# Performance work log

Hardware: AMD Instinct MI355X
Metric: run time of the kernel (lower is better)

## Reference

```python
import jax, jax.numpy as jnp
import numpy as np

B, S, NX, H = 8, 1024, 1024, 16
HD = NX // H  # head dim = 64
MASKED_BIAS = -10000.0


def setup_inputs() -> dict:
    key = jax.random.key(0)
    ks = jax.random.split(key, 6)
    return {
        "x": jax.random.normal(ks[0], (B, S, NX), dtype=jnp.float32),
        "query": jax.random.normal(ks[1], (B, S, NX), dtype=jnp.float32),
        "c_attn_w": jax.random.normal(ks[2], (NX, 3 * NX), dtype=jnp.float32) * 0.02,
        "c_attn_b": jnp.zeros((3 * NX,), dtype=jnp.float32),
        "c_proj_w": jax.random.normal(ks[3], (NX, NX), dtype=jnp.float32) * 0.02,
        "c_proj_b": jnp.zeros((NX,), dtype=jnp.float32),
    }


def _split_heads(t):
    # [B, S, NX] -> [B, H, S, HD]
    b, s, _ = t.shape
    return t.reshape(b, s, H, HD).transpose(0, 2, 1, 3)


def reference(x, query, c_attn_w, c_attn_b, c_proj_w, c_proj_b):
    # Conv1D: y = x @ W + b
    kv = x @ c_attn_w + c_attn_b          # [B,S,3NX]; use key/value slices
    qy = query @ c_attn_w + c_attn_b      # [B,S,3NX]; use query slice
    q = _split_heads(qy[..., :NX])                     # [B,H,S,HD]
    k = _split_heads(kv[..., NX:2 * NX])               # [B,H,S,HD]
    v = _split_heads(kv[..., 2 * NX:])                 # [B,H,S,HD]

    w = jnp.einsum("bhqd,bhkd->bhqk", q, k) / jnp.sqrt(jnp.float32(HD))
    causal = jnp.tril(jnp.ones((S, S), dtype=bool))[None, None]
    w = jnp.where(causal, w, jnp.float32(MASKED_BIAS))
    w = jax.nn.softmax(w, axis=-1)
    a = jnp.einsum("bhqk,bhkd->bhqd", w, v)            # [B,H,S,HD]
    a = a.transpose(0, 2, 1, 3).reshape(B, S, NX)      # merge heads
    return a @ c_proj_w + c_proj_b
```

## Files before the change

kernel.cpp:

```cpp
#include <hip/hip_runtime.h>
#include <cstdint>
#include <cstddef>

#define Bb   8
#define Ss   1024
#define NXx  1024
#define Hh   16
#define HDd  64
#define Mm   (Bb*Ss)

typedef __bf16 bf16x8 __attribute__((ext_vector_type(8)));
typedef float  f32x4  __attribute__((ext_vector_type(4)));

__device__ __forceinline__ unsigned short f2bf(float f) {
    union { float f; unsigned int u; } v; v.f = f;
    return (unsigned short)((v.u + 0x8000u) >> 16);
}
__device__ __forceinline__ unsigned int f2bf_hi(float f) {
    union { float f; unsigned int u; } v; v.f = f;
    return (v.u + 0x8000u) & 0xffff0000u;
}

__device__ __forceinline__ void load_lds16(const unsigned short* g, unsigned short* lds_base) {
    __builtin_amdgcn_global_load_lds(
        (const __attribute__((address_space(1))) void*)g,
        (__attribute__((address_space(3))) void*)lds_base, 16, 0, 0);
}

__global__ __launch_bounds__(256) void prep(
    const float* __restrict__ x, const float* __restrict__ query,
    const float* __restrict__ caw, const float* __restrict__ cpw,
    unsigned short* __restrict__ xb, unsigned short* __restrict__ qb,
    unsigned short* __restrict__ Wt, unsigned short* __restrict__ Pt)
{
    __shared__ float tile[32][33];
    const int bid = blockIdx.x;
    const int tid = threadIdx.x;

    if (bid < 16384) {
        const float* in = (bid < 8192) ? x : query;
        unsigned short* out = (bid < 8192) ? xb : qb;
        const int i = ((bid & 8191) * 256 + tid) * 4;
        const float4 v = *(const float4*)(in + i);
        unsigned long long p = (unsigned long long)f2bf(v.x)
            | ((unsigned long long)f2bf(v.y) << 16)
            | ((unsigned long long)f2bf(v.z) << 32)
            | ((unsigned long long)f2bf(v.w) << 48);
        *(unsigned long long*)(out + i) = p;
        return;
    }

    const float* in;
    unsigned short* out;
    int C, t;
    if (bid < 16384 + 3072) { in = caw; out = Wt; C = 3072; t = bid - 16384; }
    else                    { in = cpw; out = Pt; C = 1024; t = bid - 19456; }
    const int ntx = C >> 5;
    const int c0 = (t % ntx) * 32, r0 = (t / ntx) * 32;
    const int tx = tid & 31, ty = tid >> 5;
    for (int i = ty; i < 32; i += 8)
        tile[i][tx] = in[(size_t)(r0 + i) * C + c0 + tx];
    __syncthreads();
    for (int i = ty; i < 32; i += 8)
        out[(size_t)(c0 + i) * 1024 + r0 + tx] = f2bf(tile[tx][i]);
}

__global__ __launch_bounds__(256) void gemm128(
    const unsigned short* __restrict__ Ax,
    const unsigned short* __restrict__ Aq,
    const unsigned short* __restrict__ Bt,
    const float* __restrict__ bias,
    int K, int mode,
    unsigned short* __restrict__ out_q,
    unsigned short* __restrict__ out_k,
    unsigned short* __restrict__ out_v,
    float* __restrict__ out_f)
{
    __shared__ unsigned short smem[16384];
    unsigned short (*As)[64] = (unsigned short (*)[64])(smem);
    unsigned short (*Bs)[64] = (unsigned short (*)[64])(smem + 8192);

    const int tid  = threadIdx.x;
    const int w    = tid >> 6;
    const int lane = tid & 63;

    const int nx   = (mode == 0) ? 24 : 8;
    const int nxh  = nx >> 1;
    const int n    = blockIdx.x;
    const int xcd  = n & 7;
    const int sgrp = n >> 3;
    const int m0   = ((xcd >> 1) * 16 + sgrp / nxh) * 128;
    const int n0   = ((xcd & 1) * nxh + sgrp % nxh) * 128;
    const int region = n0 >> 10;
    const unsigned short* A = (mode == 0 && region == 0) ? Aq : Ax;

    const int wm   = (w >> 1) * 64;
    const int wn   = (w & 1) * 64;
    const int lrow = lane & 15;
    const int quad = lane >> 4;

    f32x4 acc[4][4] = {};

    const int rr   = lane >> 3;
    const int scol = (((lane & 7) ^ (lane >> 3)) << 3);
    const unsigned short* Ag = A  + (size_t)(m0 + w * 32 + rr) * K + scol;
    const unsigned short* Bg = Bt + (size_t)(n0 + w * 32 + rr) * K + scol;
    unsigned short* ldsA = smem + (w * 32) * 64;
    unsigned short* ldsB = smem + 8192 + (w * 32) * 64;

    const int swz = lrow & 7;

    for (int k0 = 0; k0 < K; k0 += 64) {
        __syncthreads();
#pragma unroll
        for (int c = 0; c < 4; ++c) {
            load_lds16(Ag + (size_t)(c * 8) * K + k0, ldsA + c * 512);
            load_lds16(Bg + (size_t)(c * 8) * K + k0, ldsB + c * 512);
        }
        __syncthreads();
#pragma unroll
        for (int kk = 0; kk < 2; ++kk) {
            bf16x8 af[4], bfr[4];
            const int pc = (((kk * 4 + quad) ^ swz) << 3);
#pragma unroll
            for (int i = 0; i < 4; ++i) {
                af[i]  = *(const bf16x8*)&As[wm + i * 16 + lrow][pc];
                bfr[i] = *(const bf16x8*)&Bs[wn + i * 16 + lrow][pc];
            }
#pragma unroll
            for (int i = 0; i < 4; ++i)
#pragma unroll
                for (int j = 0; j < 4; ++j)
                    acc[i][j] = __builtin_amdgcn_mfma_f32_16x16x32_bf16(af[i], bfr[j], acc[i][j], 0, 0, 0);
        }
    }

    __syncthreads();

    if (mode == 1) {
#pragma unroll
        for (int i = 0; i < 4; ++i)
#pragma unroll
            for (int j = 0; j < 4; ++j) {
                const int ncol = n0 + wn + j * 16 + lrow;
                const float bv = bias[ncol];
#pragma unroll
                for (int r = 0; r < 4; ++r) {
                    const int mrow = m0 + wm + i * 16 + quad * 4 + r;
                    out_f[(size_t)mrow * NXx + ncol] = acc[i][j][r] + bv;
                }
            }
        return;
    }

    unsigned short* ep = smem + w * 2048;

    if (region != 2) {
        unsigned short* outp = (region == 0) ? out_q : out_k;
#pragma unroll
        for (int j = 0; j < 4; ++j) {
            const float bv = bias[n0 + wn + j * 16 + lrow];
#pragma unroll
            for (int i = 0; i < 4; ++i)
#pragma unroll
                for (int r = 0; r < 4; ++r)
                    ep[(i * 16 + quad * 4 + r) * 24 + lrow] = f2bf(acc[i][j][r] + bv);
#pragma unroll
            for (int t = 0; t < 2; ++t) {
                const int c    = t * 64 + lane;
                const int row  = c >> 1, ch = (c & 1) * 8;
                const int mrow = m0 + wm + row;
                const int cc   = (n0 + wn + j * 16 + ch) & (NXx - 1);
                const int hh   = cc >> 6, dd = cc & 63;
                const int bh   = (mrow >> 10) * Hh + hh;
                const int ss   = mrow & (Ss - 1);
                *(uint4*)&outp[((size_t)bh * Ss + ss) * HDd + dd] =
                    *(const uint4*)&ep[row * 24 + ch];
            }
        }
    } else {
#pragma unroll
        for (int j = 0; j < 4; ++j) {
            const float bv = bias[n0 + wn + j * 16 + lrow];
#pragma unroll
            for (int i = 0; i < 4; ++i)
#pragma unroll
                for (int r = 0; r < 4; ++r)
                    ep[lrow * 72 + i * 16 + quad * 4 + r] = f2bf(acc[i][j][r] + bv);
#pragma unroll
            for (int t = 0; t < 2; ++t) {
                const int c    = t * 64 + lane;
                const int col  = c >> 3, rc = (c & 7) * 8;
                const int cc   = (n0 + wn + j * 16 + col) & (NXx - 1);
                const int hh   = cc >> 6, dd = cc & 63;
                const int mrow = m0 + wm + rc;
                const int bh   = (mrow >> 10) * Hh + hh;
                const int ss   = mrow & (Ss - 1);
                *(uint4*)&out_v[((size_t)bh * HDd + dd) * Ss + ss] =
                    *(const uint4*)&ep[col * 72 + rc];
            }
        }
    }
}

__global__ __launch_bounds__(512, 2) void gemm256(
    const unsigned short* __restrict__ Ax,
    const unsigned short* __restrict__ Aq,
    const unsigned short* __restrict__ Bt,
    const float* __restrict__ bias,
    unsigned short* __restrict__ out_q,
    unsigned short* __restrict__ out_k,
    unsigned short* __restrict__ out_v)
{
    __shared__ unsigned short lds[49152];

    const int tid  = threadIdx.x;
    const int w    = tid >> 6;
    const int lane = tid & 63;
    const int wm   = (w >> 2) * 128;
    const int wn   = (w & 3) * 32;
    const int lrow = lane & 15;
    const int quad = lane >> 4;
    const int swz  = lrow & 7;
    const int ca   = (quad ^ swz) << 3;
    const int cb   = ((4 + quad) ^ swz) << 3;

    const int n    = blockIdx.x;
    const int xcd  = n & 7;
    const int sg   = n >> 3;
    const int mi   = (xcd >> 1) * 8 + (sg & 7);
    const int ni   = (xcd & 1) * 12 + (sg >> 3);
    const int m0   = mi << 8;
    const int n0   = ni << 7;
    const int region = n0 >> 10;
    const unsigned short* A = (region == 0) ? Aq : Ax;

    const int srow = lane >> 3;
    const int chnk = (((lane & 7) ^ srow) << 3);
    const unsigned short* pA0 = A  + (size_t)(m0 +       w * 8 + srow) * 1024 + chnk;
    const unsigned short* pA1 = A  + (size_t)(m0 +  64 + w * 8 + srow) * 1024 + chnk;
    const unsigned short* pA2 = A  + (size_t)(m0 + 128 + w * 8 + srow) * 1024 + chnk;
    const unsigned short* pA3 = A  + (size_t)(m0 + 192 + w * 8 + srow) * 1024 + chnk;
    const unsigned short* pB0 = Bt + (size_t)(n0 +       w * 8 + srow) * 1024 + chnk;
    const unsigned short* pB1 = Bt + (size_t)(n0 +  64 + w * 8 + srow) * 1024 + chnk;
    const int wl = w * 512;

    f32x4 acc[8][2] = {};

    load_lds16(pA0, lds + 0 * 4096 + wl);
    load_lds16(pA2, lds + 2 * 4096 + wl);
    load_lds16(pB0, lds + 32768 + 0 * 4096 + wl);
    load_lds16(pB1, lds + 32768 + 1 * 4096 + wl);
    load_lds16(pA1, lds + 1 * 4096 + wl);
    load_lds16(pA3, lds + 3 * 4096 + wl);
    pA0 += 64; pA1 += 64; pA2 += 64; pA3 += 64;
    pB0 += 64; pB1 += 64;

    asm volatile("s_waitcnt vmcnt(2)" ::: "memory");
    __builtin_amdgcn_s_barrier();
    asm volatile("" ::: "memory");

#pragma unroll 1
    for (int t = 0; t < 16; ++t) {
        const int ab = (t & 1) * 16384;
        const int bb = 32768 + (t & 1) * 8192;
        const int ua = ((t & 1) ^ 1) * 16384;
        const int ub = 32768 + ((t & 1) ^ 1) * 8192;
        const bool st = (t < 15);
        const int rbA = ab + (wm + lrow) * 64;
        const int rbB = bb + (wn + lrow) * 64;

        bf16x8 a0f[4], a1f[4], b0q[2], b1q[2];

#pragma unroll
        for (int i = 0; i < 4; ++i) {
            a0f[i] = *(const bf16x8*)&lds[rbA + i * 1024 + ca];
            a1f[i] = *(const bf16x8*)&lds[rbA + i * 1024 + cb];
        }
#pragma unroll
        for (int j = 0; j < 2; ++j) {
            b0q[j] = *(const bf16x8*)&lds[rbB + j * 1024 + ca];
            b1q[j] = *(const bf16x8*)&lds[rbB + j * 1024 + cb];
        }
        if (st) {
            load_lds16(pA0, lds + ua + 0 * 4096 + wl);
            load_lds16(pA2, lds + ua + 2 * 4096 + wl);
            load_lds16(pB0, lds + ub + 0 * 4096 + wl);
            load_lds16(pB1, lds + ub + 1 * 4096 + wl);
        }
        __builtin_amdgcn_s_barrier();
        asm volatile("s_waitcnt lgkmcnt(0)" ::: "memory");
        __builtin_amdgcn_s_setprio(1);
#pragma unroll
        for (int i = 0; i < 4; ++i)
#pragma unroll
            for (int j = 0; j < 2; ++j)
                acc[i][j] = __builtin_amdgcn_mfma_f32_16x16x32_bf16(a0f[i], b0q[j], acc[i][j], 0, 0, 0);
#pragma unroll
        for (int i = 0; i < 4; ++i)
#pragma unroll
            for (int j = 0; j < 2; ++j)
                acc[i][j] = __builtin_amdgcn_mfma_f32_16x16x32_bf16(a1f[i], b1q[j], acc[i][j], 0, 0, 0);
        __builtin_amdgcn_s_setprio(0);
        if (st) asm volatile("s_waitcnt vmcnt(4)" ::: "memory");
        else    asm volatile("s_waitcnt vmcnt(0)" ::: "memory");
        asm volatile("" ::: "memory");
        __builtin_amdgcn_s_barrier();
        asm volatile("" ::: "memory");

#pragma unroll
        for (int i = 0; i < 4; ++i) {
            a0f[i] = *(const bf16x8*)&lds[rbA + 4096 + i * 1024 + ca];
            a1f[i] = *(const bf16x8*)&lds[rbA + 4096 + i * 1024 + cb];
        }
        if (st) {
            load_lds16(pA1, lds + ua + 1 * 4096 + wl);
            load_lds16(pA3, lds + ua + 3 * 4096 + wl);
            pA0 += 64; pA1 += 64; pA2 += 64; pA3 += 64;
            pB0 += 64; pB1 += 64;
        }
        __builtin_amdgcn_s_barrier();
        asm volatile("s_waitcnt lgkmcnt(0)" ::: "memory");
        __builtin_amdgcn_s_setprio(1);
#pragma unroll
        for (int i = 0; i < 4; ++i)
#pragma unroll
            for (int j = 0; j < 2; ++j)
                acc[4 + i][j] = __builtin_amdgcn_mfma_f32_16x16x32_bf16(a0f[i], b0q[j], acc[4 + i][j], 0, 0, 0);
#pragma unroll
        for (int i = 0; i < 4; ++i)
#pragma unroll
            for (int j = 0; j < 2; ++j)
                acc[4 + i][j] = __builtin_amdgcn_mfma_f32_16x16x32_bf16(a1f[i], b1q[j], acc[4 + i][j], 0, 0, 0);
        __builtin_amdgcn_s_setprio(0);
        if (st) asm volatile("s_waitcnt vmcnt(2)" ::: "memory");
        asm volatile("" ::: "memory");
        __builtin_amdgcn_s_barrier();
        asm volatile("" ::: "memory");
    }

    __syncthreads();

    unsigned short* ep = lds + w * 6144;

    if (region != 2) {
        unsigned short* outp = (region == 0) ? out_q : out_k;
#pragma unroll
        for (int j = 0; j < 2; ++j) {
            const float bv = bias[n0 + wn + j * 16 + lrow];
#pragma unroll
            for (int i = 0; i < 8; ++i)
#pragma unroll
                for (int r = 0; r < 4; ++r)
                    ep[(i * 16 + quad * 4 + r) * 24 + lrow] = f2bf(acc[i][j][r] + bv);
#pragma unroll
            for (int tt = 0; tt < 4; ++tt) {
                const int c    = tt * 64 + lane;
                const int row  = c >> 1, ch = (c & 1) * 8;
                const int mrow = m0 + wm + row;
                const int cc   = (n0 + wn + j * 16 + ch) & (NXx - 1);
                const int hh   = cc >> 6, dd = cc & 63;
                const int bh   = (mrow >> 10) * Hh + hh;
                const int ss   = mrow & (Ss - 1);
                *(uint4*)&outp[((size_t)bh * Ss + ss) * HDd + dd] =
                    *(const uint4*)&ep[row * 24 + ch];
            }
        }
    } else {
#pragma unroll
        for (int j = 0; j < 2; ++j) {
            const float bv = bias[n0 + wn + j * 16 + lrow];
#pragma unroll
            for (int i = 0; i < 8; ++i)
#pragma unroll
                for (int r = 0; r < 4; ++r)
                    ep[lrow * 136 + i * 16 + quad * 4 + r] = f2bf(acc[i][j][r] + bv);
#pragma unroll
            for (int tt = 0; tt < 4; ++tt) {
                const int c    = tt * 64 + lane;
                const int col  = c >> 4, rc = (c & 15) * 8;
                const int cc   = (n0 + wn + j * 16 + col) & (NXx - 1);
                const int hh   = cc >> 6, dd = cc & 63;
                const int mrow = m0 + wm + rc;
                const int bh   = (mrow >> 10) * Hh + hh;
                const int ss   = mrow & (Ss - 1);
                *(uint4*)&out_v[((size_t)bh * HDd + dd) * Ss + ss] =
                    *(const uint4*)&ep[col * 136 + rc];
            }
        }
    }
}

__global__ __launch_bounds__(256) void flash_attn(
    const unsigned short* __restrict__ Qh,
    const unsigned short* __restrict__ Kh,
    const unsigned short* __restrict__ Vt,
    unsigned short* __restrict__ about)
{
    __shared__ unsigned short Ks[64][64];
    __shared__ unsigned short Vs[64][64];
    __shared__ unsigned short Pl[4][32][72];

    const int tid  = threadIdx.x;
    const int w    = tid >> 6;
    const int lane = tid & 63;
    const int bh   = blockIdx.x & 127;
    const int pr   = blockIdx.x >> 7;
    const int b    = bh >> 4, h = bh & 15;
    const int lrow = lane & 15;
    const int quad = lane >> 4;

    const unsigned short* Qb = Qh + (size_t)bh * Ss * HDd;
    const unsigned short* Kb = Kh + (size_t)bh * Ss * HDd;
    const unsigned short* Vb = Vt + (size_t)bh * HDd * Ss;

    const int sr = lane >> 3;
    const int lc = (((lane & 7) ^ (lane >> 3)) << 3);
    unsigned short* ldsK0 = &Ks[w * 16][0];
    unsigned short* ldsK1 = &Ks[w * 16 + 8][0];
    unsigned short* ldsV0 = &Vs[w * 16][0];
    unsigned short* ldsV1 = &Vs[w * 16 + 8][0];

    const int swz = lrow & 7;
    const int ca = ((quad ^ swz) << 3);
    const int cb = (((4 + quad) ^ swz) << 3);

    for (int half = 0; half < 2; ++half) {
        const int qt = half ? (7 - pr) : pr;
        const int qw = qt * 128 + w * 32;

        bf16x8 aq[2][2];
#pragma unroll
        for (int g = 0; g < 2; ++g)
#pragma unroll
            for (int c = 0; c < 2; ++c)
                aq[g][c] = *(const bf16x8*)(Qb + (size_t)(qw + g * 16 + lrow) * HDd + c * 32 + quad * 8);

        f32x4 O[2][4] = {};
        float lsum[2] = { 0.f, 0.f };

        const int nkt = 2 * qt + 2;
        for (int kt = 0; kt < nkt; ++kt) {
            const int k0 = kt * 64;

            __syncthreads();
            load_lds16(Kb + (size_t)(k0 + w * 16 + sr) * HDd + lc,     ldsK0);
            load_lds16(Kb + (size_t)(k0 + w * 16 + sr + 8) * HDd + lc, ldsK1);
            load_lds16(Vb + (size_t)(w * 16 + sr) * Ss + k0 + lc,      ldsV0);
            load_lds16(Vb + (size_t)(w * 16 + sr + 8) * Ss + k0 + lc,  ldsV1);
            __syncthreads();

            if (k0 > qw + 31) continue;

            f32x4 st[2][4] = {};
#pragma unroll
            for (int j = 0; j < 4; ++j) {
                const bf16x8 kf0 = *(const bf16x8*)&Ks[j * 16 + lrow][ca];
                const bf16x8 kf1 = *(const bf16x8*)&Ks[j * 16 + lrow][cb];
                st[0][j] = __builtin_amdgcn_mfma_f32_16x16x32_bf16(kf0, aq[0][0], st[0][j], 0, 0, 0);
                st[0][j] = __builtin_amdgcn_mfma_f32_16x16x32_bf16(kf1, aq[0][1], st[0][j], 0, 0, 0);
                st[1][j] = __builtin_amdgcn_mfma_f32_16x16x32_bf16(kf0, aq[1][0], st[1][j], 0, 0, 0);
                st[1][j] = __builtin_amdgcn_mfma_f32_16x16x32_bf16(kf1, aq[1][1], st[1][j], 0, 0, 0);
            }

            const bool needMask = (k0 + 63 > qw);
#pragma unroll
            for (int g = 0; g < 2; ++g) {
                const int qg = qw + g * 16 + lrow;
#pragma unroll
                for (int j = 0; j < 4; ++j) {
                    const int kbase = k0 + j * 16 + quad * 4;
                    float e0 = __expf(st[g][j][0] * 0.125f);
                    float e1 = __expf(st[g][j][1] * 0.125f);
                    float e2 = __expf(st[g][j][2] * 0.125f);
                    float e3 = __expf(st[g][j][3] * 0.125f);
                    if (needMask) {
                        if (kbase     > qg) e0 = 0.f;
                        if (kbase + 1 > qg) e1 = 0.f;
                        if (kbase + 2 > qg) e2 = 0.f;
                        if (kbase + 3 > qg) e3 = 0.f;
                    }
                    lsum[g] += (e0 + e1) + (e2 + e3);
                    uint2 pk;
                    pk.x = (unsigned)f2bf(e0) | f2bf_hi(e1);
                    pk.y = (unsigned)f2bf(e2) | f2bf_hi(e3);
                    *(uint2*)&Pl[w][g * 16 + lrow][j * 16 + quad * 4] = pk;
                }
            }

            bf16x8 ap[2][2];
#pragma unroll
            for (int g = 0; g < 2; ++g)
#pragma unroll
                for (int c = 0; c < 2; ++c)
                    ap[g][c] = *(const bf16x8*)&Pl[w][g * 16 + lrow][c * 32 + quad * 8];
#pragma unroll
            for (int f = 0; f < 4; ++f) {
                const bf16x8 vf0 = *(const bf16x8*)&Vs[f * 16 + lrow][ca];
                const bf16x8 vf1 = *(const bf16x8*)&Vs[f * 16 + lrow][cb];
                O[0][f] = __builtin_amdgcn_mfma_f32_16x16x32_bf16(ap[0][0], vf0, O[0][f], 0, 0, 0);
                O[0][f] = __builtin_amdgcn_mfma_f32_16x16x32_bf16(ap[0][1], vf1, O[0][f], 0, 0, 0);
                O[1][f] = __builtin_amdgcn_mfma_f32_16x16x32_bf16(ap[1][0], vf0, O[1][f], 0, 0, 0);
                O[1][f] = __builtin_amdgcn_mfma_f32_16x16x32_bf16(ap[1][1], vf1, O[1][f], 0, 0, 0);
            }
        }

#pragma unroll
        for (int g = 0; g < 2; ++g) {
            float l = lsum[g];
            l += __shfl_xor(l, 16);
            l += __shfl_xor(l, 32);
            const float inv = 1.0f / l;
#pragma unroll
            for (int r = 0; r < 4; ++r) {
                const float invr = __shfl(inv, quad * 4 + r);
                const int q = qw + g * 16 + quad * 4 + r;
                const size_t base = ((size_t)b * Ss + q) * NXx + h * HDd;
#pragma unroll
                for (int f = 0; f < 4; ++f)
                    about[base + f * 16 + lrow] = f2bf(O[g][f][r] * invr);
            }
        }
    }
}

extern "C" void kernel_launch(void* const* d_in, const int* in_sizes, int n_in,
                              void* d_out, int out_size, void* d_ws, size_t ws_size,
                              hipStream_t stream) {
    const float* x        = (const float*)d_in[0];
    const float* query    = (const float*)d_in[1];
    const float* c_attn_w = (const float*)d_in[2];
    const float* c_attn_b = (const float*)d_in[3];
    const float* c_proj_w = (const float*)d_in[4];
    const float* c_proj_b = (const float*)d_in[5];
    float* out = (float*)d_out;

    const size_t nTok = (size_t)Mm * NXx;
    char* ws = (char*)d_ws;
    unsigned short* xb    = (unsigned short*)ws;                 ws += nTok * 2;
    unsigned short* qb    = (unsigned short*)ws;                 ws += nTok * 2;
    unsigned short* Wt    = (unsigned short*)ws;                 ws += (size_t)3 * NXx * NXx * 2;
    unsigned short* Pt    = (unsigned short*)ws;                 ws += (size_t)NXx * NXx * 2;
    unsigned short* Qh    = (unsigned short*)ws;                 ws += nTok * 2;
    unsigned short* Kh    = (unsigned short*)ws;                 ws += nTok * 2;
    unsigned short* Vt    = (unsigned short*)ws;                 ws += nTok * 2;
    unsigned short* about = (unsigned short*)ws;                 ws += nTok * 2;
    if ((size_t)(ws - (char*)d_ws) > ws_size) return;

    prep<<<20480, 256, 0, stream>>>(x, query, c_attn_w, c_proj_w, xb, qb, Wt, Pt);

    gemm256<<<768, 512, 0, stream>>>(xb, qb, Wt, c_attn_b, Qh, Kh, Vt);

    flash_attn<<<512, 256, 0, stream>>>(Qh, Kh, Vt, about);

    gemm128<<<dim3(8 * 64), 256, 0, stream>>>(about, nullptr, Pt, c_proj_b, NXx, 1,
                                              nullptr, nullptr, nullptr, out);
}
```

Baseline: 255.9 us.

## Triple-buffer QKV GEMM K-loop and retile warps to 64x64

Changes the 256x128 QKV projection GEMM from a double-buffered, half-step pipeline to a triple-buffered pipeline that prefetches two K-steps ahead with one barrier pair per step. Each warp now computes a 64x64 subtile (4x4 MFMA fragments) instead of 128x32, which changes operand reuse per LDS read. The block-to-tile mapping order also changes for L2 locality. LDS use grows from 96KB to 144KB per block. That likely drops occupancy from two blocks per CU to one, trading latency hiding across blocks for deeper prefetch within a block.

```diff
diff --git a/kernel.cpp b/kernel.cpp
--- a/kernel.cpp
+++ b/kernel.cpp
@@ -212,13 +212,13 @@
     unsigned short* __restrict__ out_k,
     unsigned short* __restrict__ out_v)
 {
-    __shared__ unsigned short lds[49152];
+    __shared__ unsigned short lds[73728];
 
     const int tid  = threadIdx.x;
     const int w    = tid >> 6;
     const int lane = tid & 63;
-    const int wm   = (w >> 2) * 128;
-    const int wn   = (w & 3) * 32;
+    const int wm   = (w >> 1) * 64;
+    const int wn   = (w & 1) * 64;
     const int lrow = lane & 15;
     const int quad = lane >> 4;
     const int swz  = lrow & 7;
@@ -228,8 +228,8 @@
     const int n    = blockIdx.x;
     const int xcd  = n & 7;
     const int sg   = n >> 3;
-    const int mi   = (xcd >> 1) * 8 + (sg & 7);
-    const int ni   = (xcd & 1) * 12 + (sg >> 3);
+    const int mi   = (xcd >> 1) * 8 + sg / 12;
+    const int ni   = (xcd & 1) * 12 + sg % 12;
     const int m0   = mi << 8;
     const int n0   = ni << 7;
     const int region = n0 >> 10;
@@ -245,116 +245,90 @@
     const unsigned short* pB1 = Bt + (size_t)(n0 +  64 + w * 8 + srow) * 1024 + chnk;
     const int wl = w * 512;
 
-    f32x4 acc[8][2] = {};
-
-    load_lds16(pA0, lds + 0 * 4096 + wl);
-    load_lds16(pA2, lds + 2 * 4096 + wl);
-    load_lds16(pB0, lds + 32768 + 0 * 4096 + wl);
-    load_lds16(pB1, lds + 32768 + 1 * 4096 + wl);
-    load_lds16(pA1, lds + 1 * 4096 + wl);
-    load_lds16(pA3, lds + 3 * 4096 + wl);
-    pA0 += 64; pA1 += 64; pA2 += 64; pA3 += 64;
-    pB0 += 64; pB1 += 64;
-
-    asm volatile("s_waitcnt vmcnt(2)" ::: "memory");
-    __builtin_amdgcn_s_barrier();
-    asm volatile("" ::: "memory");
-
+    f32x4 acc[4][4] = {};
+
+#pragma unroll
+    for (int p = 0; p < 2; ++p) {
+        const int bb = p * 24576;
+        load_lds16(pA0, lds + bb + 0 * 4096 + wl);
+        load_lds16(pA1, lds + bb + 1 * 4096 + wl);
+        load_lds16(pA2, lds + bb + 2 * 4096 + wl);
+        load_lds16(pA3, lds + bb + 3 * 4096 + wl);
+        load_lds16(pB0, lds + bb + 16384 + 0 * 4096 + wl);
+        load_lds16(pB1, lds + bb + 16384 + 1 * 4096 + wl);
+        pA0 += 64; pA1 += 64; pA2 += 64; pA3 += 64; pB0 += 64; pB1 += 64;
+    }
+
+    int cbuf = 0;
+    int sbuf = 2;
 #pragma unroll 1
     for (int t = 0; t < 16; ++t) {
-        const int ab = (t & 1) * 16384;
-        const int bb = 32768 + (t & 1) * 8192;
-        const int ua = ((t & 1) ^ 1) * 16384;
-        const int ub = 32768 + ((t & 1) ^ 1) * 8192;
-        const bool st = (t < 15);
-        const int rbA = ab + (wm + lrow) * 64;
-        const int rbB = bb + (wn + lrow) * 64;
-
-        bf16x8 a0f[4], a1f[4], b0q[2], b1q[2];
-
+        __builtin_amdgcn_s_barrier();
+        asm volatile("" ::: "memory");
+        if (t <= 13) {
+            const int bb = sbuf * 24576;
+            load_lds16(pA0, lds + bb + 0 * 4096 + wl);
+            load_lds16(pA1, lds + bb + 1 * 4096 + wl);
+            load_lds16(pA2, lds + bb + 2 * 4096 + wl);
+            load_lds16(pA3, lds + bb + 3 * 4096 + wl);
+            load_lds16(pB0, lds + bb + 16384 + 0 * 4096 + wl);
+            load_lds16(pB1, lds + bb + 16384 + 1 * 4096 + wl);
+            pA0 += 64; pA1 += 64; pA2 += 64; pA3 += 64; pB0 += 64; pB1 += 64;
+            asm volatile("s_waitcnt vmcnt(12)" ::: "memory");
+        } else if (t == 14) {
+            asm volatile("s_waitcnt vmcnt(6)" ::: "memory");
+        } else {
+            asm volatile("s_waitcnt vmcnt(0)" ::: "memory");
+        }
+        __builtin_amdgcn_s_barrier();
+        asm volatile("" ::: "memory");
+
+        const int rbA = cbuf * 24576 + (wm + lrow) * 64;
+        const int rbB = cbuf * 24576 + 16384 + (wn + lrow) * 64;
+        bf16x8 a0f[4], a1f[4], b0q[4], b1q[4];
 #pragma unroll
         for (int i = 0; i < 4; ++i) {
             a0f[i] = *(const bf16x8*)&lds[rbA + i * 1024 + ca];
             a1f[i] = *(const bf16x8*)&lds[rbA + i * 1024 + cb];
         }
 #pragma unroll
-        for (int j = 0; j < 2; ++j) {
+        for (int j = 0; j < 4; ++j) {
             b0q[j] = *(const bf16x8*)&lds[rbB + j * 1024 + ca];
             b1q[j] = *(const bf16x8*)&lds[rbB + j * 1024 + cb];
         }
-        if (st) {
-            load_lds16(pA0, lds + ua + 0 * 4096 + wl);
-            load_lds16(pA2, lds + ua + 2 * 4096 + wl);
-            load_lds16(pB0, lds + ub + 0 * 4096 + wl);
-            load_lds16(pB1, lds + ub + 1 * 4096 + wl);
-        }
-        __builtin_amdgcn_s_barrier();
-        asm volatile("s_waitcnt lgkmcnt(0)" ::: "memory");
         __builtin_amdgcn_s_setprio(1);
 #pragma unroll
         for (int i = 0; i < 4; ++i)
 #pragma unroll
-            for (int j = 0; j < 2; ++j)
+            for (int j = 0; j < 4; ++j)
                 acc[i][j] = __builtin_amdgcn_mfma_f32_16x16x32_bf16(a0f[i], b0q[j], acc[i][j], 0, 0, 0);
 #pragma unroll
         for (int i = 0; i < 4; ++i)
 #pragma unroll
-            for (int j = 0; j < 2; ++j)
+            for (int j = 0; j < 4; ++j)
                 acc[i][j] = __builtin_amdgcn_mfma_f32_16x16x32_bf16(a1f[i], b1q[j], acc[i][j], 0, 0, 0);
         __builtin_amdgcn_s_setprio(0);
-        if (st) asm volatile("s_waitcnt vmcnt(4)" ::: "memory");
-        else    asm volatile("s_waitcnt vmcnt(0)" ::: "memory");
-        asm volatile("" ::: "memory");
-        __builtin_amdgcn_s_barrier();
-        asm volatile("" ::: "memory");
-
-#pragma unroll
-        for (int i = 0; i < 4; ++i) {
-            a0f[i] = *(const bf16x8*)&lds[rbA + 4096 + i * 1024 + ca];
-            a1f[i] = *(const bf16x8*)&lds[rbA + 4096 + i * 1024 + cb];
-        }
-        if (st) {
-            load_lds16(pA1, lds + ua + 1 * 4096 + wl);
-            load_lds16(pA3, lds + ua + 3 * 4096 + wl);
-            pA0 += 64; pA1 += 64; pA2 += 64; pA3 += 64;
-            pB0 += 64; pB1 += 64;
-        }
-        __builtin_amdgcn_s_barrier();
-        asm volatile("s_waitcnt lgkmcnt(0)" ::: "memory");
-        __builtin_amdgcn_s_setprio(1);
-#pragma unroll
-        for (int i = 0; i < 4; ++i)
-#pragma unroll
-            for (int j = 0; j < 2; ++j)
-                acc[4 + i][j] = __builtin_amdgcn_mfma_f32_16x16x32_bf16(a0f[i], b0q[j], acc[4 + i][j], 0, 0, 0);
-#pragma unroll
-        for (int i = 0; i < 4; ++i)
-#pragma unroll
-            for (int j = 0; j < 2; ++j)
-                acc[4 + i][j] = __builtin_amdgcn_mfma_f32_16x16x32_bf16(a1f[i], b1q[j], acc[4 + i][j], 0, 0, 0);
-        __builtin_amdgcn_s_setprio(0);
-        if (st) asm volatile("s_waitcnt vmcnt(2)" ::: "memory");
-        asm volatile("" ::: "memory");
-        __builtin_amdgcn_s_barrier();
-        asm volatile("" ::: "memory");
+
+        cbuf = (cbuf == 2) ? 0 : cbuf + 1;
+        sbuf = (sbuf == 2) ? 0 : sbuf + 1;
     }
 
     __syncthreads();
 
-    unsigned short* ep = lds + w * 6144;
+    unsigned short* ep = lds + w * 2048;
 
     if (region != 2) {
         unsigned short* outp = (region == 0) ? out_q : out_k;
 #pragma unroll
-        for (int j = 0; j < 2; ++j) {
+        for (int j = 0; j < 4; ++j) {
             const float bv = bias[n0 + wn + j * 16 + lrow];
 #pragma unroll
-            for (int i = 0; i < 8; ++i)
+            for (int i = 0; i < 4; ++i)
 #pragma unroll
                 for (int r = 0; r < 4; ++r)
                     ep[(i * 16 + quad * 4 + r) * 24 + lrow] = f2bf(acc[i][j][r] + bv);
 #pragma unroll
-            for (int tt = 0; tt < 4; ++tt) {
+            for (int tt = 0; tt < 2; ++tt) {
                 const int c    = tt * 64 + lane;
                 const int row  = c >> 1, ch = (c & 1) * 8;
                 const int mrow = m0 + wm + row;
@@ -368,24 +342,24 @@
         }
     } else {
 #pragma unroll
-        for (int j = 0; j < 2; ++j) {
+        for (int j = 0; j < 4; ++j) {
             const float bv = bias[n0 + wn + j * 16 + lrow];
 #pragma unroll
-            for (int i = 0; i < 8; ++i)
+            for (int i = 0; i < 4; ++i)
 #pragma unroll
                 for (int r = 0; r < 4; ++r)
-                    ep[lrow * 136 + i * 16 + quad * 4 + r] = f2bf(acc[i][j][r] + bv);
-#pragma unroll
-            for (int tt = 0; tt < 4; ++tt) {
+                    ep[lrow * 72 + i * 16 + quad * 4 + r] = f2bf(acc[i][j][r] + bv);
+#pragma unroll
+            for (int tt = 0; tt < 2; ++tt) {
                 const int c    = tt * 64 + lane;
-                const int col  = c >> 4, rc = (c & 15) * 8;
+                const int col  = c >> 3, rc = (c & 7) * 8;
                 const int cc   = (n0 + wn + j * 16 + col) & (NXx - 1);
                 const int hh   = cc >> 6, dd = cc & 63;
                 const int mrow = m0 + wm + rc;
                 const int bh   = (mrow >> 10) * Hh + hh;
                 const int ss   = mrow & (Ss - 1);
                 *(uint4*)&out_v[((size_t)bh * HDd + dd) * Ss + ss] =
-                    *(const uint4*)&ep[col * 136 + rc];
+                    *(const uint4*)&ep[col * 72 + rc];
             }
         }
     }
```

Measured after the change: 260.0 us. No clear change (+1.6%).
